# Optimization experiments

Hardware: AMD Instinct MI355X
Metric: run time of the kernel (lower is better)

Reference implementation:

```python
import jax, jax.numpy as jnp
import numpy as np
import math

B, S, D = 4, 2048, 1024
H = 16
HD = D // H  # 64
NEG_INF = -1e9


def setup_inputs() -> dict:
    key = jax.random.key(0)
    k1, k2, k3, k4, k5 = jax.random.split(key, 5)
    x = jax.random.normal(k1, (B, S, D), dtype=jnp.float32)
    # rotary frequencies (theta = 10000), shape (S, HD//2)
    inv_freq = 1.0 / (10000.0 ** (jnp.arange(0, HD, 2, dtype=jnp.float32) / HD))
    t = jnp.arange(S, dtype=jnp.float32)
    freqs = jnp.outer(t, inv_freq)  # (S, HD//2)
    freqs_cos = jnp.cos(freqs)
    freqs_sin = jnp.sin(freqs)
    # causal additive mask (1,1,S,S)
    causal = jnp.tril(jnp.ones((S, S), dtype=bool))
    mask = jnp.where(causal, 0.0, NEG_INF).astype(jnp.float32)[None, None]
    scale = 0.02
    wq = jax.random.normal(k2, (D, D), dtype=jnp.float32) * scale
    wk = jax.random.normal(k3, (D, D), dtype=jnp.float32) * scale
    wv = jax.random.normal(k4, (D, D), dtype=jnp.float32) * scale
    wo = jax.random.normal(k5, (D, D), dtype=jnp.float32) * scale
    return {"x": x, "freqs_cos": freqs_cos, "freqs_sin": freqs_sin,
            "mask": mask, "wq": wq, "wk": wk, "wv": wv, "wo": wo}


def _apply_rotary(t, cos, sin):
    # t: (B,S,H,HD); cos/sin: (S, HD//2) broadcast as (1,S,1,HD//2)
    tr = t.reshape(*t.shape[:-1], HD // 2, 2)
    t0, t1 = tr[..., 0], tr[..., 1]
    c = cos[None, :, None, :]
    s = sin[None, :, None, :]
    o0 = t0 * c - t1 * s
    o1 = t0 * s + t1 * c
    return jnp.stack([o0, o1], axis=-1).reshape(t.shape)


def reference(x, freqs_cos, freqs_sin, mask, wq, wk, wv, wo):
    bsz, seqlen, _ = x.shape
    xq = (x @ wq).reshape(bsz, seqlen, H, HD)
    xk = (x @ wk).reshape(bsz, seqlen, H, HD)
    xv = (x @ wv).reshape(bsz, seqlen, H, HD)
    xq = _apply_rotary(xq, freqs_cos, freqs_sin)
    xk = _apply_rotary(xk, freqs_cos, freqs_sin)
    # (B,H,S,HD)
    xq = xq.transpose(0, 2, 1, 3)
    xk = xk.transpose(0, 2, 1, 3)
    xv = xv.transpose(0, 2, 1, 3)
    scores = jnp.einsum('bhqd,bhkd->bhqk', xq, xk) / math.sqrt(HD)
    scores = scores + mask
    probs = jax.nn.softmax(scores.astype(jnp.float32), axis=-1).astype(xq.dtype)
    # dropout is identity in eval mode
    out = jnp.einsum('bhqk,bhkd->bhqd', probs, xv)
    out = out.transpose(0, 2, 1, 3).reshape(bsz, seqlen, H * HD)
    return out @ wo
```

## Files before the change

### kernel.cpp

```cpp
#include <hip/hip_runtime.h>
#include <stdint.h>

typedef short short8 __attribute__((ext_vector_type(8)));
typedef float f32x4 __attribute__((ext_vector_type(4)));
typedef float f32x16 __attribute__((ext_vector_type(16)));
typedef unsigned int u32x4 __attribute__((ext_vector_type(4)));
typedef float float4e __attribute__((ext_vector_type(4)));
typedef unsigned short u16;

#define BB 4
#define SS 2048
#define DD 1024
#define HH 16
#define MM (BB*SS)

__device__ __forceinline__ u16 f2bf(float f) {
    unsigned u = __float_as_uint(f);
    u += 0x7FFFu + ((u >> 16) & 1u);
    return (u16)(u >> 16);
}
__device__ __forceinline__ float bf2f(u16 h) {
    return __uint_as_float(((unsigned)h) << 16);
}
__device__ __forceinline__ unsigned cvtpk(float a, float b) {
    unsigned r;
    asm("v_cvt_pk_bf16_f32 %0, %1, %2" : "=v"(r) : "v"(a), "v"(b));
    return r;
}
__device__ __forceinline__ void gload16(const void* g, void* l) {
    __builtin_amdgcn_global_load_lds(
        (const __attribute__((address_space(1))) unsigned int*)(uintptr_t)g,
        (__attribute__((address_space(3))) unsigned int*)(unsigned)(uintptr_t)l,
        16, 0, 0);
}
__device__ __forceinline__ bool tens_is_bf(const u16* mref) { return mref[1] == 0xCE6Eu; }

__global__ __launch_bounds__(256) void cvt_x(const void* xin, u16* xb, const u16* mref) {
    bool isbf = tens_is_bf(mref);
    size_t i = (size_t)blockIdx.x * 256 + threadIdx.x;
    if (isbf) {
        ((u32x4*)xb)[i] = ((const u32x4*)xin)[i];
    } else {
        const float4e* src = (const float4e*)xin;
        float4e a = src[2*i], b = src[2*i+1];
        u32x4 o;
        o[0] = (unsigned)f2bf(a[0]) | ((unsigned)f2bf(a[1]) << 16);
        o[1] = (unsigned)f2bf(a[2]) | ((unsigned)f2bf(a[3]) << 16);
        o[2] = (unsigned)f2bf(b[0]) | ((unsigned)f2bf(b[1]) << 16);
        o[3] = (unsigned)f2bf(b[2]) | ((unsigned)f2bf(b[3]) << 16);
        ((u32x4*)xb)[i] = o;
    }
}

__global__ __launch_bounds__(256) void trw(const void* w0, const void* w1, const void* w2, const void* w3,
                                           u16* wt, const u16* mref) {
    bool isbf = tens_is_bf(mref);
    const void* w = (blockIdx.z == 0) ? w0 : (blockIdx.z == 1) ? w1 : (blockIdx.z == 2) ? w2 : w3;
    u16* out = wt + (size_t)blockIdx.z * (DD*DD);
    __shared__ float t[32][33];
    int tx = threadIdx.x & 31, ty = threadIdx.x >> 5;
    int n0 = blockIdx.x * 32, k0 = blockIdx.y * 32;
#pragma unroll
    for (int i = 0; i < 4; ++i) {
        int k = k0 + ty*4 + i;
        float v = isbf ? bf2f(((const u16*)w)[(size_t)k*DD + n0 + tx])
                       : ((const float*)w)[(size_t)k*DD + n0 + tx];
        t[ty*4 + i][tx] = v;
    }
    __syncthreads();
#pragma unroll
    for (int i = 0; i < 4; ++i)
        out[(size_t)(n0 + ty*4 + i)*DD + k0 + tx] = f2bf(t[tx][ty*4 + i]);
}

#define QSCALE 0.1803368801111204f
template<int MODE>
__global__ __launch_bounds__(256) void gemm128(const u16* __restrict__ A, const u16* __restrict__ Bt,
                                               u16* outQ, u16* outK, u16* outVT, void* Cout,
                                               const void* fcos, const void* fsin,
                                               const u16* mref) {
    constexpr int SMEMB = (MODE == 1) ? 36864 : 32768;
    __shared__ __align__(16) unsigned char smem[SMEMB];
    int tid = threadIdx.x;
    int w = tid >> 6, l = tid & 63, lo = l & 15, hi = l >> 4;
    int wm = w >> 1, wn = w & 1;
    int m0 = blockIdx.x * 128, n0 = blockIdx.y * 128;

    f32x4 acc[4][4] = {};

    auto stage = [&](int buf, int t) {
        int k0 = t * 32;
#pragma unroll
        for (int i = 0; i < 2; ++i) {
            int o = (i*256 + tid) * 16;
            int row = o >> 6, inb = o & 63;
            int sw  = inb ^ ((row & 3) << 4);
            gload16((const char*)A + ((size_t)(m0 + row)*DD + k0)*2 + sw,
                    smem + buf*16384 + (i*256 + (tid & ~63))*16);
            gload16((const char*)Bt + ((size_t)(n0 + row)*DD + k0)*2 + sw,
                    smem + buf*16384 + 8192 + (i*256 + (tid & ~63))*16);
        }
    };

    stage(0, 0);
    __syncthreads();
    int cur = 0;
    const int NT = DD / 32;
    for (int t = 0; t < NT; ++t) {
        if (t + 1 < NT) stage(cur ^ 1, t + 1);
        const char* Ab = (const char*)(smem + cur*16384);
        const char* Bb = Ab + 8192;
        short8 af[4], bfr[4];
#pragma unroll
        for (int mi = 0; mi < 4; ++mi) {
            int r = wm*64 + mi*16 + lo;
            int ib = hi * 16;
            af[mi] = *(const short8*)(Ab + r*64 + (ib ^ ((r & 3) << 4)));
        }
#pragma unroll
        for (int ni = 0; ni < 4; ++ni) {
            int r = wn*64 + ni*16 + lo;
            int ib = hi * 16;
            bfr[ni] = *(const short8*)(Bb + r*64 + (ib ^ ((r & 3) << 4)));
        }
        __builtin_amdgcn_s_setprio(1);
#pragma unroll
        for (int mi = 0; mi < 4; ++mi)
#pragma unroll
            for (int ni = 0; ni < 4; ++ni)
                acc[mi][ni] = __builtin_amdgcn_mfma_f32_16x16x32_bf16(af[mi], bfr[ni], acc[mi][ni], 0, 0, 0);
        __builtin_amdgcn_s_setprio(0);
        __syncthreads();
        cur ^= 1;
    }

    if (MODE == 1) {
        int wi = n0 >> 10;
        int n0w = n0 & 1023;
        if (wi == 2) {
            __syncthreads();
            u16* vs = (u16*)smem + w * (64*72);
#pragma unroll
            for (int ni = 0; ni < 4; ++ni) {
                int d = ni*16 + lo;
#pragma unroll
                for (int mi = 0; mi < 4; ++mi)
#pragma unroll
                    for (int rr = 0; rr < 2; ++rr) {
                        unsigned pk = (unsigned)f2bf(acc[mi][ni][2*rr]) | ((unsigned)f2bf(acc[mi][ni][2*rr+1]) << 16);
                        *(unsigned*)(vs + d*72 + mi*16 + hi*4 + rr*2) = pk;
                    }
            }
            asm volatile("s_waitcnt lgkmcnt(0)" ::: "memory");
            int bq = (m0 + wm*64) >> 11;
            int s_base = (m0 + wm*64) & (SS-1);
            int h = (n0w + wn*64) >> 6;
#pragma unroll
            for (int p = 0; p < 8; ++p) {
                int idx = p*64 + l;
                int row = idx >> 3, ch = idx & 7;
                short8 vv = *(const short8*)(vs + row*72 + ch*8);
                *(short8*)(outVT + (((size_t)bq*HH + h)*64 + row)*SS + s_base + ch*8) = vv;
            }
        } else {
            bool fbf = (((const u16*)fcos)[0] == 0x3F80u);
            u16* outp = wi ? outK : outQ;
            float oscale = wi ? 1.0f : QSCALE;
#pragma unroll
            for (int mi = 0; mi < 4; ++mi)
#pragma unroll
                for (int ni = 0; ni < 4; ++ni)
#pragma unroll
                    for (int r = 0; r < 4; ++r) {
                        int gm = m0 + wm*64 + mi*16 + hi*4 + r;
                        int gc = n0w + wn*64 + ni*16 + lo;
                        float v  = acc[mi][ni][r];
                        float vp = __shfl_xor(v, 1);
                        int s = gm & (SS-1), d = gc & 63, i2 = d >> 1;
                        float co, sn;
                        if (fbf) { co = bf2f(((const u16*)fcos)[s*32 + i2]); sn = bf2f(((const u16*)fsin)[s*32 + i2]); }
                        else     { co = ((const float*)fcos)[s*32 + i2];     sn = ((const float*)fsin)[s*32 + i2]; }
                        float o = (gc & 1) ? (vp*sn + v*co) : (v*co - vp*sn);
                        o *= oscale;
                        int b = gm >> 11, h = gc >> 6;
                        outp[((((size_t)b*HH + h)*SS + s) << 6) + d] = f2bf(o);
                    }
        }
    } else {
        bool isbf = tens_is_bf(mref);
#pragma unroll
        for (int mi = 0; mi < 4; ++mi)
#pragma unroll
            for (int ni = 0; ni < 4; ++ni)
#pragma unroll
                for (int r = 0; r < 4; ++r) {
                    int gm = m0 + wm*64 + mi*16 + hi*4 + r;
                    int gc = n0 + wn*64 + ni*16 + lo;
                    float v = acc[mi][ni][r];
                    if (isbf) ((u16*)Cout)[(size_t)gm*DD + gc] = f2bf(v);
                    else      ((float*)Cout)[(size_t)gm*DD + gc] = v;
                }
    }
}

__global__ __launch_bounds__(256) void attn(const u16* __restrict__ Q, const u16* __restrict__ K,
                                            const u16* __restrict__ VT, u16* __restrict__ AO) {
    __shared__ __align__(16) u16 Kl[2][64*64];
    __shared__ __align__(16) u16 Vl[2][64*64];
    int bh = blockIdx.x;
    int qt = (gridDim.y - 1) - blockIdx.y;
    int tid = threadIdx.x, w = tid >> 6, l = tid & 63;
    int l31 = l & 31, hi5 = l >> 5;
    const u16* Qb = Q  + (size_t)bh * SS * 64;
    const u16* Kb = K  + (size_t)bh * SS * 64;
    const u16* Vb = VT + (size_t)bh * 64 * SS;
    int q0w = qt*128 + w*32;
    int q   = q0w + l31;

    short8 qf[4];
#pragma unroll
    for (int kc = 0; kc < 4; ++kc)
        qf[kc] = *(const short8*)(Qb + (size_t)q*64 + kc*16 + hi5*8);

    int loff[2][4];
#pragma unroll
    for (int g = 0; g < 2; ++g)
#pragma unroll
        for (int kc = 0; kc < 4; ++kc) {
            int row = g*32 + l31;
            int ib = kc*32 + hi5*16;
            loff[g][kc] = row*128 + (ib ^ ((row & 7) << 4));
        }

    f32x16 oacc[2] = {};
    float m_ = -1e30f, l_ = 0.f;

    auto stage = [&](int buf, int kt) {
        const char* Kt = (const char*)(Kb + (size_t)kt*64*64);
        const char* Vt = (const char*)Vb + (size_t)kt*128;
#pragma unroll
        for (int i = 0; i < 2; ++i) {
            int idx = i*256 + tid;
            int row = idx >> 3, inb = (idx & 7) * 16;
            int sw = inb ^ ((row & 7) << 4);
            gload16(Kt + row*128 + sw,            (char*)Kl[buf] + (i*256 + (tid & ~63))*16);
            gload16(Vt + (size_t)row*(SS*2) + sw, (char*)Vl[buf] + (i*256 + (tid & ~63))*16);
        }
    };

    int nkt = 2*qt + 2;
    stage(0, 0);
    __syncthreads();
    int cur = 0;

    for (int kt = 0; kt < nkt; ++kt) {
        if (kt + 1 < nkt) stage(cur ^ 1, kt + 1);

        if (kt*64 <= q0w + 31) {
            const char* Kc = (const char*)Kl[cur];
            const char* Vc = (const char*)Vl[cur];
            f32x16 sc[2] = {};
            __builtin_amdgcn_s_setprio(1);
#pragma unroll
            for (int kvt = 0; kvt < 2; ++kvt) {
                short8 kf[4];
#pragma unroll
                for (int kc = 0; kc < 4; ++kc)
                    kf[kc] = *(const short8*)(Kc + loff[kvt][kc]);
#pragma unroll
                for (int kc = 0; kc < 4; ++kc)
                    sc[kvt] = __builtin_amdgcn_mfma_f32_32x32x16_bf16(kf[kc], qf[kc], sc[kvt], 0, 0, 0);
            }
            __builtin_amdgcn_s_setprio(0);

            if (kt*64 + 63 > q0w) {
#pragma unroll
                for (int kvt = 0; kvt < 2; ++kvt)
#pragma unroll
                    for (int rg = 0; rg < 16; ++rg) {
                        int kv = kt*64 + kvt*32 + (rg & 3) + 8*(rg >> 2) + 4*hi5;
                        if (kv > q) sc[kvt][rg] = -1e9f;
                    }
            }

            float m8[8];
#pragma unroll
            for (int j = 0; j < 8; ++j)
                m8[j] = fmaxf(fmaxf(sc[0][j], sc[0][j+8]), fmaxf(sc[1][j], sc[1][j+8]));
            float mx = fmaxf(fmaxf(fmaxf(m8[0], m8[1]), fmaxf(m8[2], m8[3])),
                             fmaxf(fmaxf(m8[4], m8[5]), fmaxf(m8[6], m8[7])));
            mx = fmaxf(mx, __shfl_xor(mx, 32));
            if (!__all(mx <= m_ + 8.f)) {
                float mn = fmaxf(m_, mx);
                float al = exp2f(m_ - mn);
                m_ = mn;
                l_ *= al;
#pragma unroll
                for (int dt = 0; dt < 2; ++dt)
#pragma unroll
                    for (int rg = 0; rg < 16; ++rg) oacc[dt][rg] *= al;
            }
#pragma unroll
            for (int kvt = 0; kvt < 2; ++kvt)
#pragma unroll
                for (int rg = 0; rg < 16; ++rg)
                    sc[kvt][rg] = exp2f(sc[kvt][rg] - m_);
            float s8[8];
#pragma unroll
            for (int j = 0; j < 8; ++j)
                s8[j] = (sc[0][j] + sc[0][j+8]) + (sc[1][j] + sc[1][j+8]);
            float rs = ((s8[0] + s8[1]) + (s8[2] + s8[3])) + ((s8[4] + s8[5]) + (s8[6] + s8[7]));
            rs += __shfl_xor(rs, 32);
            l_ += rs;

            short8 pa[4];
#pragma unroll
            for (int kc = 0; kc < 4; ++kc) {
                const int kvt = kc >> 1;
                const int base = (kc & 1) * 8;
                unsigned A0 = cvtpk(sc[kvt][base + 0], sc[kvt][base + 1]);
                unsigned A1 = cvtpk(sc[kvt][base + 2], sc[kvt][base + 3]);
                unsigned B0 = cvtpk(sc[kvt][base + 4], sc[kvt][base + 5]);
                unsigned B1 = cvtpk(sc[kvt][base + 6], sc[kvt][base + 7]);
                asm("v_permlane32_swap_b32 %0, %1" : "+v"(A0), "+v"(B0));
                asm("v_permlane32_swap_b32 %0, %1" : "+v"(A1), "+v"(B1));
                u32x4 pk; pk[0] = A0; pk[1] = A1; pk[2] = B0; pk[3] = B1;
                pa[kc] = __builtin_bit_cast(short8, pk);
            }

            __builtin_amdgcn_s_setprio(1);
#pragma unroll
            for (int dt = 0; dt < 2; ++dt) {
                short8 vf[4];
#pragma unroll
                for (int kc = 0; kc < 4; ++kc)
                    vf[kc] = *(const short8*)(Vc + loff[dt][kc]);
#pragma unroll
                for (int kc = 0; kc < 4; ++kc)
                    oacc[dt] = __builtin_amdgcn_mfma_f32_32x32x16_bf16(vf[kc], pa[kc], oacc[dt], 0, 0, 0);
            }
            __builtin_amdgcn_s_setprio(0);
        }

        __syncthreads();
        cur ^= 1;
    }

    int b = bh >> 4, h = bh & 15;
    float inv = 1.0f / l_;
    u16* aor = AO + (size_t)(b*SS + q)*DD + h*64;
#pragma unroll
    for (int dt = 0; dt < 2; ++dt)
#pragma unroll
        for (int j = 0; j < 8; ++j) {
            int r0 = 2*j, r1 = 2*j + 1;
            int d = dt*32 + (r0 & 3) + 8*(r0 >> 2) + 4*hi5;
            unsigned pk = (unsigned)f2bf(oacc[dt][r0] * inv) | ((unsigned)f2bf(oacc[dt][r1] * inv) << 16);
            *(unsigned*)(aor + d) = pk;
        }
}

extern "C" void kernel_launch(void* const* d_in, const int* in_sizes, int n_in,
                              void* d_out, int out_size, void* d_ws, size_t ws_size,
                              hipStream_t stream) {
    const void* x    = d_in[0];
    const void* fcos = d_in[1];
    const void* fsin = d_in[2];
    const u16*  mref = (const u16*)d_in[3];
    const void* wq   = d_in[4];
    const void* wk   = d_in[5];
    const void* wv   = d_in[6];
    const void* wo   = d_in[7];

    u16* ws = (u16*)d_ws;
    const size_t XB = (size_t)MM * DD;
    const size_t WT = (size_t)DD * DD;
    u16* xb  = ws;
    u16* wt  = ws + XB;
    u16* qb  = ws + XB + 4*WT;
    u16* kb  = qb + XB;
    u16* vtb = kb + XB;

    cvt_x<<<4096, 256, 0, stream>>>(x, xb, mref);
    trw<<<dim3(32, 32, 4), 256, 0, stream>>>(wq, wk, wv, wo, wt, mref);
    gemm128<1><<<dim3(64, 24), 256, 0, stream>>>(xb, wt, qb, kb, vtb, nullptr, fcos, fsin, mref);
    attn<<<dim3(64, 16), 256, 0, stream>>>(qb, kb, vtb, xb);
    gemm128<3><<<dim3(64, 8), 256, 0, stream>>>(xb, wt + 3*WT, nullptr, nullptr, nullptr, d_out, fcos, fsin, mref);
}
```

Baseline: 199.8 us.

## Use 256x256 tiled 512-thread kernel for fused QKV projection with rotary epilogue

Replaces the 128x128 QKV GEMM with a dedicated 256x256-tile kernel using 8 waves, K-step 64, 128-byte rows with XOR swizzle, and prefetch loads interleaved with the MFMA sub-steps. Larger tiles raise arithmetic intensity and cut global/LDS traffic per flop. The V-transpose epilogue now writes 4-element packed stores directly instead of staging through shared memory, which may give less coalesced writes. The grid shrinks to 384 blocks with 64KB+ LDS each, so wave-level occupancy and tail balance across CUs may change.

```diff
diff --git a/kernel.cpp b/kernel.cpp
--- a/kernel.cpp
+++ b/kernel.cpp
@@ -5,6 +5,7 @@
 typedef float f32x4 __attribute__((ext_vector_type(4)));
 typedef float f32x16 __attribute__((ext_vector_type(16)));
 typedef unsigned int u32x4 __attribute__((ext_vector_type(4)));
+typedef unsigned int u32x2 __attribute__((ext_vector_type(2)));
 typedef float float4e __attribute__((ext_vector_type(4)));
 typedef unsigned short u16;
 
@@ -74,13 +75,142 @@
 }
 
 #define QSCALE 0.1803368801111204f
-template<int MODE>
-__global__ __launch_bounds__(256) void gemm128(const u16* __restrict__ A, const u16* __restrict__ Bt,
-                                               u16* outQ, u16* outK, u16* outVT, void* Cout,
-                                               const void* fcos, const void* fsin,
-                                               const u16* mref) {
-    constexpr int SMEMB = (MODE == 1) ? 36864 : 32768;
-    __shared__ __align__(16) unsigned char smem[SMEMB];
+
+__global__ __launch_bounds__(512, 2) void qkv256(const u16* __restrict__ A, const u16* __restrict__ Bt,
+                                                 u16* __restrict__ outQ, u16* __restrict__ outK,
+                                                 u16* __restrict__ outVT,
+                                                 const void* fcos, const void* fsin) {
+    __shared__ __align__(16) u16 Al[2][256*64];
+    __shared__ __align__(16) u16 Bl[2][256*64];
+    int tid = threadIdx.x;
+    int w = tid >> 6, l = tid & 63, lo = l & 15, hi = l >> 4;
+    int wr = w >> 2, wc = w & 3;
+    int m0 = blockIdx.x * 256, n0 = blockIdx.y * 256;
+
+    f32x4 acc[8][4] = {};
+
+    auto stageA = [&](int buf, int t, int h) {
+        const char* src = (const char*)(A + ((size_t)(m0 + h*128) * DD + t*64));
+        char* dst = (char*)Al[buf] + h*128*128;
+#pragma unroll
+        for (int i = 0; i < 2; ++i) {
+            int idx = i*512 + tid;
+            int row = idx >> 3, inb = (idx & 7) * 16;
+            int sw = inb ^ ((row & 7) << 4);
+            gload16(src + (size_t)row*(DD*2) + sw, dst + (i*512 + (tid & ~63))*16);
+        }
+    };
+    auto stageB = [&](int buf, int t, int h) {
+        const char* src = (const char*)(Bt + ((size_t)(n0 + h*128) * DD + t*64));
+        char* dst = (char*)Bl[buf] + h*128*128;
+#pragma unroll
+        for (int i = 0; i < 2; ++i) {
+            int idx = i*512 + tid;
+            int row = idx >> 3, inb = (idx & 7) * 16;
+            int sw = inb ^ ((row & 7) << 4);
+            gload16(src + (size_t)row*(DD*2) + sw, dst + (i*512 + (tid & ~63))*16);
+        }
+    };
+
+    const int NT = DD / 64;
+    stageA(0, 0, 0); stageB(0, 0, 0);
+    stageA(0, 0, 1); stageB(0, 0, 1);
+    asm volatile("s_waitcnt vmcnt(0)" ::: "memory");
+    __builtin_amdgcn_s_barrier();
+
+    for (int t = 0; t < NT; ++t) {
+        int buf = t & 1, nbuf = buf ^ 1;
+        bool pre = (t + 1 < NT);
+        const char* Ab = (const char*)Al[buf];
+        const char* Bb = (const char*)Bl[buf];
+
+        short8 bfr[4][2];
+
+#pragma unroll
+        for (int j = 0; j < 4; ++j) {
+            if (j == 0 && pre) { stageA(nbuf, t+1, 0); stageB(nbuf, t+1, 0); }
+            if (j == 1 && pre) { stageA(nbuf, t+1, 1); stageB(nbuf, t+1, 1); }
+            if (j == 0) {
+#pragma unroll
+                for (int ni = 0; ni < 4; ++ni) {
+                    int lrow = wc*64 + ni*16 + lo;
+#pragma unroll
+                    for (int ks = 0; ks < 2; ++ks)
+                        bfr[ni][ks] = *(const short8*)(Bb + lrow*128 + ((ks*64 + hi*16) ^ ((lrow & 7) << 4)));
+                }
+            }
+            short8 af[2][2];
+#pragma unroll
+            for (int mm = 0; mm < 2; ++mm) {
+                int lrow = wr*128 + (2*j + mm)*16 + lo;
+#pragma unroll
+                for (int ks = 0; ks < 2; ++ks)
+                    af[mm][ks] = *(const short8*)(Ab + lrow*128 + ((ks*64 + hi*16) ^ ((lrow & 7) << 4)));
+            }
+            __builtin_amdgcn_s_barrier();
+            __builtin_amdgcn_s_setprio(1);
+#pragma unroll
+            for (int ks = 0; ks < 2; ++ks)
+#pragma unroll
+                for (int mm = 0; mm < 2; ++mm)
+#pragma unroll
+                    for (int ni = 0; ni < 4; ++ni)
+                        acc[2*j + mm][ni] = __builtin_amdgcn_mfma_f32_16x16x32_bf16(af[mm][ks], bfr[ni][ks], acc[2*j + mm][ni], 0, 0, 0);
+            __builtin_amdgcn_s_setprio(0);
+            if (j == 3) {
+                if (pre) asm volatile("s_waitcnt vmcnt(0)" ::: "memory");
+            }
+            __builtin_amdgcn_s_barrier();
+        }
+    }
+
+    int wi = n0 >> 10;
+    int n0w = n0 & 1023;
+    if (wi == 2) {
+        int gc = n0w + wc*64;
+#pragma unroll
+        for (int ni = 0; ni < 4; ++ni) {
+            int col = gc + ni*16 + lo;
+            int d = col & 63, h = col >> 6;
+#pragma unroll
+            for (int mi = 0; mi < 8; ++mi) {
+                int srow = m0 + wr*128 + mi*16 + hi*4;
+                int b = srow >> 11, s0 = srow & (SS-1);
+                u32x2 pk;
+                pk[0] = cvtpk(acc[mi][ni][0], acc[mi][ni][1]);
+                pk[1] = cvtpk(acc[mi][ni][2], acc[mi][ni][3]);
+                *(u32x2*)(outVT + ((size_t)(b*HH + h)*64 + d)*SS + s0) = pk;
+            }
+        }
+    } else {
+        bool fbf = (((const u16*)fcos)[0] == 0x3F80u);
+        u16* outp = wi ? outK : outQ;
+        float oscale = wi ? 1.0f : QSCALE;
+#pragma unroll
+        for (int mi = 0; mi < 8; ++mi)
+#pragma unroll
+            for (int ni = 0; ni < 4; ++ni)
+#pragma unroll
+                for (int r = 0; r < 4; ++r) {
+                    int gm = m0 + wr*128 + mi*16 + hi*4 + r;
+                    int gc = n0w + wc*64 + ni*16 + lo;
+                    float v  = acc[mi][ni][r];
+                    float vp = __shfl_xor(v, 1);
+                    int s = gm & (SS-1), d = gc & 63, i2 = d >> 1;
+                    float co, sn;
+                    if (fbf) { co = bf2f(((const u16*)fcos)[s*32 + i2]); sn = bf2f(((const u16*)fsin)[s*32 + i2]); }
+                    else     { co = ((const float*)fcos)[s*32 + i2];     sn = ((const float*)fsin)[s*32 + i2]; }
+                    float o = (gc & 1) ? (vp*sn + v*co) : (v*co - vp*sn);
+                    o *= oscale;
+                    int b = gm >> 11, h = gc >> 6;
+                    outp[((((size_t)b*HH + h)*SS + s) << 6) + d] = f2bf(o);
+                }
+    }
+}
+
+__global__ __launch_bounds__(256) void proj128(const u16* __restrict__ A, const u16* __restrict__ Bt,
+                                               void* Cout, const u16* mref) {
+    __shared__ __align__(16) unsigned char smem[32768];
     int tid = threadIdx.x;
     int w = tid >> 6, l = tid & 63, lo = l & 15, hi = l >> 4;
     int wm = w >> 1, wn = w & 1;
@@ -114,14 +244,12 @@
 #pragma unroll
         for (int mi = 0; mi < 4; ++mi) {
             int r = wm*64 + mi*16 + lo;
-            int ib = hi * 16;
-            af[mi] = *(const short8*)(Ab + r*64 + (ib ^ ((r & 3) << 4)));
+            af[mi] = *(const short8*)(Ab + r*64 + ((hi*16) ^ ((r & 3) << 4)));
         }
 #pragma unroll
         for (int ni = 0; ni < 4; ++ni) {
             int r = wn*64 + ni*16 + lo;
-            int ib = hi * 16;
-            bfr[ni] = *(const short8*)(Bb + r*64 + (ib ^ ((r & 3) << 4)));
+            bfr[ni] = *(const short8*)(Bb + r*64 + ((hi*16) ^ ((r & 3) << 4)));
         }
         __builtin_amdgcn_s_setprio(1);
 #pragma unroll
@@ -134,73 +262,19 @@
         cur ^= 1;
     }
 
-    if (MODE == 1) {
-        int wi = n0 >> 10;
-        int n0w = n0 & 1023;
-        if (wi == 2) {
-            __syncthreads();
-            u16* vs = (u16*)smem + w * (64*72);
-#pragma unroll
-            for (int ni = 0; ni < 4; ++ni) {
-                int d = ni*16 + lo;
-#pragma unroll
-                for (int mi = 0; mi < 4; ++mi)
-#pragma unroll
-                    for (int rr = 0; rr < 2; ++rr) {
-                        unsigned pk = (unsigned)f2bf(acc[mi][ni][2*rr]) | ((unsigned)f2bf(acc[mi][ni][2*rr+1]) << 16);
-                        *(unsigned*)(vs + d*72 + mi*16 + hi*4 + rr*2) = pk;
-                    }
-            }
-            asm volatile("s_waitcnt lgkmcnt(0)" ::: "memory");
-            int bq = (m0 + wm*64) >> 11;
-            int s_base = (m0 + wm*64) & (SS-1);
-            int h = (n0w + wn*64) >> 6;
-#pragma unroll
-            for (int p = 0; p < 8; ++p) {
-                int idx = p*64 + l;
-                int row = idx >> 3, ch = idx & 7;
-                short8 vv = *(const short8*)(vs + row*72 + ch*8);
-                *(short8*)(outVT + (((size_t)bq*HH + h)*64 + row)*SS + s_base + ch*8) = vv;
-            }
-        } else {
-            bool fbf = (((const u16*)fcos)[0] == 0x3F80u);
-            u16* outp = wi ? outK : outQ;
-            float oscale = wi ? 1.0f : QSCALE;
-#pragma unroll
-            for (int mi = 0; mi < 4; ++mi)
-#pragma unroll
-                for (int ni = 0; ni < 4; ++ni)
-#pragma unroll
-                    for (int r = 0; r < 4; ++r) {
-                        int gm = m0 + wm*64 + mi*16 + hi*4 + r;
-                        int gc = n0w + wn*64 + ni*16 + lo;
-                        float v  = acc[mi][ni][r];
-                        float vp = __shfl_xor(v, 1);
-                        int s = gm & (SS-1), d = gc & 63, i2 = d >> 1;
-                        float co, sn;
-                        if (fbf) { co = bf2f(((const u16*)fcos)[s*32 + i2]); sn = bf2f(((const u16*)fsin)[s*32 + i2]); }
-                        else     { co = ((const float*)fcos)[s*32 + i2];     sn = ((const float*)fsin)[s*32 + i2]; }
-                        float o = (gc & 1) ? (vp*sn + v*co) : (v*co - vp*sn);
-                        o *= oscale;
-                        int b = gm >> 11, h = gc >> 6;
-                        outp[((((size_t)b*HH + h)*SS + s) << 6) + d] = f2bf(o);
-                    }
-        }
-    } else {
-        bool isbf = tens_is_bf(mref);
-#pragma unroll
-        for (int mi = 0; mi < 4; ++mi)
-#pragma unroll
-            for (int ni = 0; ni < 4; ++ni)
-#pragma unroll
-                for (int r = 0; r < 4; ++r) {
-                    int gm = m0 + wm*64 + mi*16 + hi*4 + r;
-                    int gc = n0 + wn*64 + ni*16 + lo;
-                    float v = acc[mi][ni][r];
-                    if (isbf) ((u16*)Cout)[(size_t)gm*DD + gc] = f2bf(v);
-                    else      ((float*)Cout)[(size_t)gm*DD + gc] = v;
-                }
-    }
+    bool isbf = tens_is_bf(mref);
+#pragma unroll
+    for (int mi = 0; mi < 4; ++mi)
+#pragma unroll
+        for (int ni = 0; ni < 4; ++ni)
+#pragma unroll
+            for (int r = 0; r < 4; ++r) {
+                int gm = m0 + wm*64 + mi*16 + hi*4 + r;
+                int gc = n0 + wn*64 + ni*16 + lo;
+                float v = acc[mi][ni][r];
+                if (isbf) ((u16*)Cout)[(size_t)gm*DD + gc] = f2bf(v);
+                else      ((float*)Cout)[(size_t)gm*DD + gc] = v;
+            }
 }
 
 __global__ __launch_bounds__(256) void attn(const u16* __restrict__ Q, const u16* __restrict__ K,
@@ -383,7 +457,7 @@
 
     cvt_x<<<4096, 256, 0, stream>>>(x, xb, mref);
     trw<<<dim3(32, 32, 4), 256, 0, stream>>>(wq, wk, wv, wo, wt, mref);
-    gemm128<1><<<dim3(64, 24), 256, 0, stream>>>(xb, wt, qb, kb, vtb, nullptr, fcos, fsin, mref);
+    qkv256<<<dim3(32, 12), 512, 0, stream>>>(xb, wt, qb, kb, vtb, fcos, fsin);
     attn<<<dim3(64, 16), 256, 0, stream>>>(qb, kb, vtb, xb);
-    gemm128<3><<<dim3(64, 8), 256, 0, stream>>>(xb, wt + 3*WT, nullptr, nullptr, nullptr, d_out, fcos, fsin, mref);
-}
+    proj128<<<dim3(64, 8), 256, 0, stream>>>(xb, wt + 3*WT, d_out, mref);
+}
```

Measured after the change: 201.0 us. Within noise of the previous version (+0.6%).
